# Kernel optimization log

Measured on AMD Instinct MI355X. Metric: run time of the kernel, lower is better.

Reference implementation:

```python
import jax, jax.numpy as jnp
import numpy as np

NUM_HEADS = 16
EPS = 1e-6
NEG_INF = -1e9


def layer_norm(x, scale, bias):
    m = jnp.mean(x, axis=-1, keepdims=True)
    v = jnp.mean(jnp.square(x - m), axis=-1, keepdims=True)
    return (x - m) * jax.lax.rsqrt(v + EPS) * scale + bias


def mha(x_q, x_kv, wq, wk, wv, wo, causal):
    B, Sq, D = x_q.shape
    Sk = x_kv.shape[1]
    H = NUM_HEADS
    Dh = D // H
    q = (x_q @ wq).reshape(B, Sq, H, Dh) * (1.0 / np.sqrt(Dh))
    k = (x_kv @ wk).reshape(B, Sk, H, Dh)
    v = (x_kv @ wv).reshape(B, Sk, H, Dh)
    scores = jnp.einsum('bqhf,bkhf->bhqk', q, k)  # [B,H,Sq,Sk]
    if causal:
        mask = jnp.tril(jnp.ones((Sq, Sk), dtype=bool))
        scores = jnp.where(mask, scores, NEG_INF)
    p = jax.nn.softmax(scores, axis=-1)
    o = jnp.einsum('bhqk,bkhf->bqhf', p, v).reshape(B, Sq, D)
    return o @ wo


def setup_inputs() -> dict:
    key = jax.random.key(0)
    ks = jax.random.split(key, 12)
    B, S, D, F = 2, 2048, 1024, 4096
    w = 0.02
    return {
        'targets': jax.random.normal(ks[0], (B, S, D), jnp.float32),
        'encoded': jax.random.normal(ks[1], (B, S, D), jnp.float32),
        'ln1_s': jnp.ones((D,), jnp.float32),
        'ln1_b': jnp.zeros((D,), jnp.float32),
        'sa_wq': jax.random.normal(ks[2], (D, D), jnp.float32) * w,
        'sa_wk': jax.random.normal(ks[3], (D, D), jnp.float32) * w,
        'sa_wv': jax.random.normal(ks[4], (D, D), jnp.float32) * w,
        'sa_wo': jax.random.normal(ks[5], (D, D), jnp.float32) * w,
        'ln2_s': jnp.ones((D,), jnp.float32),
        'ln2_b': jnp.zeros((D,), jnp.float32),
        'ca_wq': jax.random.normal(ks[6], (D, D), jnp.float32) * w,
        'ca_wk': jax.random.normal(ks[7], (D, D), jnp.float32) * w,
        'ca_wv': jax.random.normal(ks[8], (D, D), jnp.float32) * w,
        'ca_wo': jax.random.normal(ks[9], (D, D), jnp.float32) * w,
        'ln3_s': jnp.ones((D,), jnp.float32),
        'ln3_b': jnp.zeros((D,), jnp.float32),
        'mlp_w1': jax.random.normal(ks[10], (D, F), jnp.float32) * w,
        'mlp_b1': jnp.zeros((F,), jnp.float32),
        'mlp_w2': jax.random.normal(ks[11], (F, D), jnp.float32) * w,
        'mlp_b2': jnp.zeros((D,), jnp.float32),
    }


def reference(targets, encoded, ln1_s, ln1_b, sa_wq, sa_wk, sa_wv, sa_wo,
              ln2_s, ln2_b, ca_wq, ca_wk, ca_wv, ca_wo,
              ln3_s, ln3_b, mlp_w1, mlp_b1, mlp_w2, mlp_b2):
    # Pre-LN causal self-attention + residual
    x = layer_norm(targets, ln1_s, ln1_b)
    x = mha(x, x, sa_wq, sa_wk, sa_wv, sa_wo, causal=True)
    x = x + targets
    # Pre-LN cross-attention over encoder output + residual
    y = layer_norm(x, ln2_s, ln2_b)
    y = mha(y, encoded, ca_wq, ca_wk, ca_wv, ca_wo, causal=False)
    y = y + x
    # Pre-LN MLP + residual
    z = layer_norm(y, ln3_s, ln3_b)
    z = jax.nn.relu(z @ mlp_w1 + mlp_b1) @ mlp_w2 + mlp_b2
    return y + z
```

## Files before the change

kernel.cpp:

```cpp
#include <hip/hip_runtime.h>


#define DEV __device__ __forceinline__

typedef __attribute__((ext_vector_type(8))) _Float16 half8;
typedef __attribute__((ext_vector_type(4))) _Float16 half4;
typedef __attribute__((ext_vector_type(2))) _Float16 half2v;
typedef __attribute__((ext_vector_type(4))) float    f32x4;
typedef __attribute__((ext_vector_type(4))) unsigned int uint4v;

#define GLB(p) ((const __attribute__((address_space(1))) void*)(p))
#define LDS(p) ((__attribute__((address_space(3))) void*)(p))

DEV half2v pk(float a, float b) {
  return __builtin_bit_cast(half2v, __builtin_amdgcn_cvt_pkrtz(a, b));
}
DEV half4 pk4(float a, float b, float c, float d) {
  half2v lo = pk(a, b), hi = pk(c, d);
  half4 r; r.x = lo.x; r.y = lo.y; r.z = hi.x; r.w = hi.y;
  return r;
}

DEV float wave_sum_f(float v) {
  #pragma unroll
  for (int off = 32; off; off >>= 1) v += __shfl_xor(v, off);
  return v;
}

struct WtArgs { const float* w[8]; _Float16* wt[8]; };

__global__ __launch_bounds__(256) void wt_square(WtArgs a) {
  const float* w = a.w[blockIdx.z];
  _Float16* wt = a.wt[blockIdx.z];
  __shared__ float t[32][33];
  const int tx = threadIdx.x, ty = threadIdx.y;
  const int n0 = blockIdx.x * 32, k0 = blockIdx.y * 32;
  #pragma unroll
  for (int i = ty; i < 32; i += 8)
    t[i][tx] = w[(size_t)(k0 + i) * 1024 + n0 + tx];
  __syncthreads();
  #pragma unroll
  for (int i = ty; i < 32; i += 8)
    wt[(size_t)(n0 + i) * 1024 + k0 + tx] = (_Float16)t[tx][i];
}

__global__ __launch_bounds__(256) void wt_one(const float* __restrict__ w,
                                              _Float16* __restrict__ wt,
                                              int K, int N) {
  __shared__ float t[32][33];
  const int tx = threadIdx.x, ty = threadIdx.y;
  const int n0 = blockIdx.x * 32, k0 = blockIdx.y * 32;
  #pragma unroll
  for (int i = ty; i < 32; i += 8)
    t[i][tx] = w[(size_t)(k0 + i) * N + n0 + tx];
  __syncthreads();
  #pragma unroll
  for (int i = ty; i < 32; i += 8)
    wt[(size_t)(n0 + i) * K + k0 + tx] = (_Float16)t[tx][i];
}

__global__ __launch_bounds__(256) void cvt_f16(const float* __restrict__ in,
                                               _Float16* __restrict__ out) {
  const size_t i = ((size_t)blockIdx.x * 256 + threadIdx.x) * 4;
  const float4 v = *(const float4*)(in + i);
  *(half4*)(out + i) = pk4(v.x, v.y, v.z, v.w);
}

__global__ __launch_bounds__(256) void ln_kernel(const float* __restrict__ x,
                                                 const float* __restrict__ sc,
                                                 const float* __restrict__ bi,
                                                 _Float16* __restrict__ out) {
  const int row = blockIdx.x;
  const int t = threadIdx.x;
  const float4 v = ((const float4*)(x + (size_t)row * 1024))[t];
  float s  = v.x + v.y + v.z + v.w;
  float s2 = v.x * v.x + v.y * v.y + v.z * v.z + v.w * v.w;
  s = wave_sum_f(s); s2 = wave_sum_f(s2);
  __shared__ float red[8];
  const int lane = t & 63, wid = t >> 6;
  if (lane == 0) { red[wid] = s; red[4 + wid] = s2; }
  __syncthreads();
  s  = red[0] + red[1] + red[2] + red[3];
  s2 = red[4] + red[5] + red[6] + red[7];
  const float mean = s * (1.f / 1024.f);
  const float rstd = rsqrtf(s2 * (1.f / 1024.f) - mean * mean + 1e-6f);
  const float4 sv = ((const float4*)sc)[t];
  const float4 bv = ((const float4*)bi)[t];
  half4 o = pk4((v.x - mean) * rstd * sv.x + bv.x,
                (v.y - mean) * rstd * sv.y + bv.y,
                (v.z - mean) * rstd * sv.z + bv.z,
                (v.w - mean) * rstd * sv.w + bv.w);
  ((half4*)(out + (size_t)row * 1024))[t] = o;
}

template <int EPI, int BM, int BN, int BK>
__global__ __launch_bounds__(256)
void gemm_f16(const _Float16* __restrict__ A, const _Float16* __restrict__ Bt,
              void* __restrict__ Cout, const float* __restrict__ bias,
              const float* __restrict__ resid, int M, int N, int K,
              float scl, int sclCols, _Float16* __restrict__ vt, int vcol0) {
  constexpr int AM = BM / 32;
  constexpr int AN = BN / 32;
  constexpr int RA = BM * BK / 2048;
  constexpr int RB = BN * BK / 2048;
  constexpr int TPR = BK / 8;
  constexpr int RPR = 2048 / BK;
  constexpr int SWM = TPR - 1;
  constexpr int SH  = (TPR == 4) ? 1 : 0;
  __shared__ _Float16 As[2][BM * BK];
  __shared__ _Float16 Bs[2][BN * BK];
  const int tid = threadIdx.x;
  const int lane = tid & 63, wid = tid >> 6;
  const int wm = wid >> 1, wn = wid & 1;
  const int q = lane >> 4, m15 = lane & 15;

  const int nwg = gridDim.x * gridDim.y;
  const int bflat = blockIdx.x + gridDim.x * blockIdx.y;
  const int swz = (bflat & 7) * (nwg >> 3) + (bflat >> 3);
  const int bn = swz % gridDim.x;
  const int bm = swz / gridDim.x;

  const int trow = tid / TPR;
  const int tcolsw = ((tid % TPR) ^ ((trow >> SH) & SWM)) * 8;
  const _Float16* Ab = A + ((size_t)bm * BM + trow) * K + tcolsw;
  const _Float16* Bb = Bt + ((size_t)bn * BN + trow) * K + tcolsw;

  f32x4 acc[AM][AN] = {};

  auto stage = [&](int k0, int buf) {
    #pragma unroll
    for (int r = 0; r < RA; r++)
      __builtin_amdgcn_global_load_lds(GLB(Ab + (size_t)r * RPR * K + k0),
                                       LDS(&As[buf][r * 2048 + wid * 512]), 16, 0, 0);
    #pragma unroll
    for (int r = 0; r < RB; r++)
      __builtin_amdgcn_global_load_lds(GLB(Bb + (size_t)r * RPR * K + k0),
                                       LDS(&Bs[buf][r * 2048 + wid * 512]), 16, 0, 0);
  };

  stage(0, 0);
  const int nit = K / BK;
  for (int it = 0; it < nit; it++) {
    const int buf = it & 1;
    __syncthreads();
    if (it + 1 < nit) stage((it + 1) * BK, buf ^ 1);
    #pragma unroll
    for (int kk = 0; kk < BK / 32; kk++) {
      half8 af[AM], bf[AN];
      #pragma unroll
      for (int i = 0; i < AM; i++) {
        const int ra = wm * (BM / 2) + i * 16 + m15;
        af[i] = *(const half8*)&As[buf][ra * BK + (((kk * 4 + q) ^ ((ra >> SH) & SWM)) << 3)];
      }
      #pragma unroll
      for (int i = 0; i < AN; i++) {
        const int rb = wn * (BN / 2) + i * 16 + m15;
        bf[i] = *(const half8*)&Bs[buf][rb * BK + (((kk * 4 + q) ^ ((rb >> SH) & SWM)) << 3)];
      }
      #pragma unroll
      for (int mi = 0; mi < AM; mi++)
        #pragma unroll
        for (int ni = 0; ni < AN; ni++)
          acc[mi][ni] = __builtin_amdgcn_mfma_f32_16x16x32_f16(af[mi], bf[ni],
                                                               acc[mi][ni], 0, 0, 0);
    }
  }

  const int rowbase = bm * BM + wm * (BM / 2);
  const int colbase = bn * BN + wn * (BN / 2);
  #pragma unroll
  for (int ni = 0; ni < AN; ni++) {
    const int col = colbase + ni * 16 + m15;
    float bv = 0.f;
    if (EPI == 2 || EPI == 4) bv = bias[col];
    const float cs = (EPI == 1 || EPI == 5) ? (col < sclCols ? scl : 1.f) : 1.f;
    if (EPI == 5 && col >= vcol0) {
      const int d = col & 63, hh = (col >> 6) & 15;
      #pragma unroll
      for (int mi = 0; mi < AM; mi++) {
        const int row = rowbase + mi * 16 + q * 4;
        const int bb = row >> 11, ss = row & 2047;
        half4 ov = pk4(acc[mi][ni][0], acc[mi][ni][1],
                       acc[mi][ni][2], acc[mi][ni][3]);
        *(half4*)(vt + ((size_t)(bb * 16 + hh) * 64 + d) * 2048 + ss) = ov;
      }
      continue;
    }
    #pragma unroll
    for (int mi = 0; mi < AM; mi++) {
      #pragma unroll
      for (int r = 0; r < 4; r++) {
        const int row = rowbase + mi * 16 + q * 4 + r;
        const size_t idx = (size_t)row * N + col;
        float v = acc[mi][ni][r];
        if (EPI == 1 || EPI == 5) {
          ((_Float16*)Cout)[idx] = (_Float16)(v * cs);
        } else if (EPI == 2) {
          v += bv; v = v > 0.f ? v : 0.f;
          ((_Float16*)Cout)[idx] = (_Float16)v;
        } else if (EPI == 3) {
          ((float*)Cout)[idx] = v + resid[idx];
        } else {
          ((float*)Cout)[idx] = v + bv + resid[idx];
        }
      }
    }
  }
}

__global__ __launch_bounds__(256, 4)
void flash_attn(const _Float16* __restrict__ Q, int qs,
                const _Float16* __restrict__ Kp, int ks,
                const _Float16* __restrict__ Vt,
                _Float16* __restrict__ Opart, float* __restrict__ Lpart,
                int S, int Sk, int causal) {
  __shared__ _Float16 Ks[2][64 * 64];
  __shared__ _Float16 Vs[2][64 * 64];
  const int tid = threadIdx.x;
  const int lane = tid & 63, wid = tid >> 6;
  const int quad = lane >> 4, c15 = lane & 15;

  const int gx = gridDim.x;
  const int lid = blockIdx.x + gx * (blockIdx.y + 16 * blockIdx.z);
  const int xcd = lid & 7, slot = lid >> 3;
  const int bh = xcd * 4 + (slot / gx);
  const int qs2 = slot % gx;
  const int h = bh & 15, b = bh >> 4;
  int qb = qs2 >> 1;
  const int split = qs2 & 1;
  const int NQB = gx >> 1;
  if (causal) qb = (qb & 1) ? (NQB - 1 - (qb >> 1)) : (qb >> 1);
  const int qw0 = qb * 128 + wid * 32;

  half8 qf[2][2];
  #pragma unroll
  for (int nt = 0; nt < 2; nt++)
    #pragma unroll
    for (int kk = 0; kk < 2; kk++)
      qf[nt][kk] = *(const half8*)(Q + (size_t)(b * S + qw0 + nt * 16 + c15) * qs +
                                   h * 64 + kk * 32 + quad * 8);

  f32x4 oacc[4][2];
  #pragma unroll
  for (int i = 0; i < 4; i++)
    #pragma unroll
    for (int j = 0; j < 2; j++)
      oacc[i][j] = (f32x4){0.f, 0.f, 0.f, 0.f};
  float lpart[2] = {0.f, 0.f};

  const int ntF = causal ? (2 * qb + 2) : (Sk >> 6);
  const _Float16* Kg = Kp + (size_t)b * Sk * ks + h * 64;
  const _Float16* Vg = Vt + (size_t)(b * 16 + h) * 64 * Sk;

  const int srow8 = lane >> 3;
  const int ssw = (((lane & 7) ^ srow8) << 3);
  auto stage = [&](int jb, int buf) {
    #pragma unroll
    for (int r = 0; r < 2; r++) {
      const int row = wid * 8 + srow8 + r * 32;
      __builtin_amdgcn_global_load_lds(
          GLB(Kg + (size_t)(jb + row) * ks + ssw),
          LDS(&Ks[buf][(wid * 8 + r * 32) * 64]), 16, 0, 0);
      __builtin_amdgcn_global_load_lds(
          GLB(Vg + (size_t)row * Sk + jb + ssw),
          LDS(&Vs[buf][(wid * 8 + r * 32) * 64]), 16, 0, 0);
    }
  };

  const int t0 = split;
  stage(t0 << 6, 0);
  __syncthreads();

  const int rsw = c15 & 7;
  const int ck0 = ((quad ^ rsw) << 3);
  const int ck1 = (((quad ^ 4) ^ rsw) << 3);

  int cur = 0;
  for (int t = t0; t < ntF; t += 2) {
    const int jb = t << 6;
    if (t + 2 < ntF) stage((t + 2) << 6, cur ^ 1);

    if (!(causal && jb > qw0 + 31)) {
      f32x4 s[4][2];
      #pragma unroll
      for (int mt = 0; mt < 4; mt++) {
        const half8 kf0 = *(const half8*)&Ks[cur][(mt * 16 + c15) * 64 + ck0];
        const half8 kf1 = *(const half8*)&Ks[cur][(mt * 16 + c15) * 64 + ck1];
        #pragma unroll
        for (int nt = 0; nt < 2; nt++) {
          f32x4 z = {0.f, 0.f, 0.f, 0.f};
          z = __builtin_amdgcn_mfma_f32_16x16x32_f16(kf0, qf[nt][0], z, 0, 0, 0);
          z = __builtin_amdgcn_mfma_f32_16x16x32_f16(kf1, qf[nt][1], z, 0, 0, 0);
          s[mt][nt] = z;
        }
      }

      if (causal && jb + 63 > qw0) {
        #pragma unroll
        for (int mt = 0; mt < 4; mt++)
          #pragma unroll
          for (int nt = 0; nt < 2; nt++) {
            const int qglob = qw0 + nt * 16 + c15;
            #pragma unroll
            for (int rr = 0; rr < 4; rr++) {
              const int kglob = jb + mt * 16 + quad * 4 + rr;
              if (kglob > qglob) s[mt][nt][rr] = -1e30f;
            }
          }
      }

      unsigned int pkd[4][2][2];
      #pragma unroll
      for (int nt = 0; nt < 2; nt++) {
        float psum = 0.f;
        #pragma unroll
        for (int mt = 0; mt < 4; mt++) {
          #pragma unroll
          for (int rr = 0; rr < 4; rr++) {
            const float p = exp2f(s[mt][nt][rr]);
            s[mt][nt][rr] = p;
            psum += p;
          }
          pkd[mt][nt][0] = __builtin_bit_cast(unsigned int,
                             pk(s[mt][nt][0], s[mt][nt][1]));
          pkd[mt][nt][1] = __builtin_bit_cast(unsigned int,
                             pk(s[mt][nt][2], s[mt][nt][3]));
        }
        lpart[nt] += psum;
      }

      half8 pb[2][2];
      #pragma unroll
      for (int kk = 0; kk < 2; kk++)
        #pragma unroll
        for (int nt = 0; nt < 2; nt++) {
          unsigned int w[4];
          #pragma unroll
          for (int jd = 0; jd < 4; jd++) {
            const int src = ((quad & 1) * 2 + (jd >> 1)) * 16 + c15;
            const unsigned int xs = __shfl(pkd[2 * kk][nt][jd & 1], src);
            const unsigned int ys = __shfl(pkd[2 * kk + 1][nt][jd & 1], src);
            w[jd] = (quad & 2) ? ys : xs;
          }
          uint4v u = {w[0], w[1], w[2], w[3]};
          pb[kk][nt] = __builtin_bit_cast(half8, u);
        }

      #pragma unroll
      for (int mtd = 0; mtd < 4; mtd++) {
        const half8 vf0 = *(const half8*)&Vs[cur][(mtd * 16 + c15) * 64 + ck0];
        const half8 vf1 = *(const half8*)&Vs[cur][(mtd * 16 + c15) * 64 + ck1];
        #pragma unroll
        for (int nt = 0; nt < 2; nt++) {
          oacc[mtd][nt] = __builtin_amdgcn_mfma_f32_16x16x32_f16(vf0, pb[0][nt],
                                                                 oacc[mtd][nt], 0, 0, 0);
          oacc[mtd][nt] = __builtin_amdgcn_mfma_f32_16x16x32_f16(vf1, pb[1][nt],
                                                                 oacc[mtd][nt], 0, 0, 0);
        }
      }
    }

    __syncthreads();
    cur ^= 1;
  }

  _Float16* Ob = Opart + (size_t)split * ((size_t)2 * S * 1024) +
                 (size_t)b * S * 1024;
  #pragma unroll
  for (int nt = 0; nt < 2; nt++) {
    float l = lpart[nt];
    l += __shfl_xor(l, 16);
    l += __shfl_xor(l, 32);
    const int qrow = qw0 + nt * 16 + c15;
    if (quad == 0)
      Lpart[((size_t)(split * 2 + b) * 16 + h) * S + qrow] = l;
    #pragma unroll
    for (int mtd = 0; mtd < 4; mtd++) {
      half4 ov = pk4(oacc[mtd][nt][0], oacc[mtd][nt][1],
                     oacc[mtd][nt][2], oacc[mtd][nt][3]);
      *(half4*)(Ob + (size_t)qrow * 1024 + h * 64 + mtd * 16 + quad * 4) = ov;
    }
  }
}

__global__ __launch_bounds__(256)
void attn_combine(const _Float16* __restrict__ Op, const float* __restrict__ Lp,
                  _Float16* __restrict__ O) {
  const int row = blockIdx.x, tid = threadIdx.x;
  const int col = tid << 2, h = tid >> 4;
  const int b = row >> 11, sq = row & 2047;
  const float la = Lp[((size_t)(b * 16 + h)) * 2048 + sq];
  const float lb = Lp[((size_t)((b + 2) * 16 + h)) * 2048 + sq];
  const float linv = 1.f / (la + lb);
  const half4 pa = *(const half4*)(Op + (size_t)row * 1024 + col);
  const half4 pb = *(const half4*)(Op + ((size_t)4096 + row) * 1024 + col);
  half4 o = pk4(((float)pa.x + (float)pb.x) * linv,
                ((float)pa.y + (float)pb.y) * linv,
                ((float)pa.z + (float)pb.z) * linv,
                ((float)pa.w + (float)pb.w) * linv);
  *(half4*)(O + (size_t)row * 1024 + col) = o;
}

extern "C" void kernel_launch(void* const* d_in, const int* in_sizes, int n_in,
                              void* d_out, int out_size, void* d_ws, size_t ws_size,
                              hipStream_t stream) {
  const float* targets = (const float*)d_in[0];
  const float* encoded = (const float*)d_in[1];
  const float* ln1_s = (const float*)d_in[2];
  const float* ln1_b = (const float*)d_in[3];
  const float* sa_wq = (const float*)d_in[4];
  const float* sa_wk = (const float*)d_in[5];
  const float* sa_wv = (const float*)d_in[6];
  const float* sa_wo = (const float*)d_in[7];
  const float* ln2_s = (const float*)d_in[8];
  const float* ln2_b = (const float*)d_in[9];
  const float* ca_wq = (const float*)d_in[10];
  const float* ca_wk = (const float*)d_in[11];
  const float* ca_wv = (const float*)d_in[12];
  const float* ca_wo = (const float*)d_in[13];
  const float* ln3_s = (const float*)d_in[14];
  const float* ln3_b = (const float*)d_in[15];
  const float* mlp_w1 = (const float*)d_in[16];
  const float* mlp_b1 = (const float*)d_in[17];
  const float* mlp_w2 = (const float*)d_in[18];
  const float* mlp_b2 = (const float*)d_in[19];

  const int B = 2, S = 2048, D = 1024, F = 4096, M = B * S;
  const size_t MB = 1024ull * 1024ull;
  const float QSCALE = 0.125f * 1.44269504f;
  char* ws = (char*)d_ws;
  _Float16* wsq   = (_Float16*)(ws);
  _Float16* w1t   = (_Float16*)(ws + 16 * MB);
  _Float16* w2t   = (_Float16*)(ws + 24 * MB);
  _Float16* Abf   = (_Float16*)(ws + 32 * MB);
  _Float16* encbf = (_Float16*)(ws + 40 * MB);
  _Float16* QKV   = (_Float16*)(ws + 48 * MB);
  _Float16* Qcb   = (_Float16*)(ws + 48 * MB);
  _Float16* KVb   = (_Float16*)(ws + 56 * MB);
  _Float16* h1    = (_Float16*)(ws + 48 * MB);
  float*    Lbuf  = (float*)(ws + 72 * MB);
  _Float16* Vtb   = (_Float16*)(ws + 80 * MB);
  _Float16* Aob   = (_Float16*)(ws + 88 * MB);
  float*    xres  = (float*)(ws + 96 * MB);
  float*    yres  = (float*)(ws + 112 * MB);
  _Float16* Opart = (_Float16*)(ws + 112 * MB);

  {
    WtArgs wa;
    const float* sw[8] = {sa_wq, sa_wk, sa_wv, sa_wo, ca_wq, ca_wk, ca_wv, ca_wo};
    for (int i = 0; i < 8; i++) { wa.w[i] = sw[i]; wa.wt[i] = wsq + (size_t)i * D * D; }
    wt_square<<<dim3(32, 32, 8), dim3(32, 8), 0, stream>>>(wa);
  }
  wt_one<<<dim3(F / 32, D / 32), dim3(32, 8), 0, stream>>>(mlp_w1, w1t, D, F);
  wt_one<<<dim3(D / 32, F / 32), dim3(32, 8), 0, stream>>>(mlp_w2, w2t, F, D);
  cvt_f16<<<(M * D) / 1024, 256, 0, stream>>>(encoded, encbf);

  const dim3 gA(2 * (S / 128), 16, B);

  ln_kernel<<<M, 256, 0, stream>>>(targets, ln1_s, ln1_b, Abf);
  gemm_f16<5, 128, 128, 32><<<dim3(3072 / 128, M / 128), 256, 0, stream>>>(
      Abf, wsq, QKV, nullptr, nullptr, M, 3072, D, QSCALE, 1024, Vtb, 2048);
  flash_attn<<<gA, 256, 0, stream>>>(QKV, 3072, QKV + 1024, 3072, Vtb,
                                     Opart, Lbuf, S, S, 1);
  attn_combine<<<M, 256, 0, stream>>>(Opart, Lbuf, Aob);
  gemm_f16<3, 64, 64, 64><<<dim3(1024 / 64, M / 64), 256, 0, stream>>>(
      Aob, wsq + 3ull * D * D, xres, nullptr, targets, M, D, D, 1.f, 0, nullptr, 0);

  ln_kernel<<<M, 256, 0, stream>>>(xres, ln2_s, ln2_b, Abf);
  gemm_f16<1, 64, 64, 64><<<dim3(1024 / 64, M / 64), 256, 0, stream>>>(
      Abf, wsq + 4ull * D * D, Qcb, nullptr, nullptr, M, D, D, QSCALE, 1024, nullptr, 0);
  gemm_f16<5, 64, 128, 32><<<dim3(2048 / 128, M / 64), 256, 0, stream>>>(
      encbf, wsq + 5ull * D * D, KVb, nullptr, nullptr, M, 2048, D, 1.f, 0, Vtb, 1024);
  flash_attn<<<gA, 256, 0, stream>>>(Qcb, 1024, KVb, 2048, Vtb,
                                     Opart, Lbuf, S, S, 0);
  attn_combine<<<M, 256, 0, stream>>>(Opart, Lbuf, Aob);
  gemm_f16<3, 64, 64, 64><<<dim3(1024 / 64, M / 64), 256, 0, stream>>>(
      Aob, wsq + 7ull * D * D, yres, nullptr, xres, M, D, D, 1.f, 0, nullptr, 0);

  ln_kernel<<<M, 256, 0, stream>>>(yres, ln3_s, ln3_b, Abf);
  gemm_f16<2, 128, 128, 32><<<dim3(F / 128, M / 128), 256, 0, stream>>>(
      Abf, w1t, h1, mlp_b1, nullptr, M, F, D, 1.f, 0, nullptr, 0);
  gemm_f16<4, 64, 64, 64><<<dim3(1024 / 64, M / 64), 256, 0, stream>>>(
      h1, w2t, (float*)d_out, mlp_b2, yres, M, D, F, 1.f, 0, nullptr, 0);

  (void)in_sizes; (void)n_in; (void)out_size; (void)ws_size;
}
```

Baseline: 540.2 us.

## Use 512-thread attention blocks with 256-row query tiles and three-way KV split

```diff
diff --git a/kernel.cpp b/kernel.cpp
--- a/kernel.cpp
+++ b/kernel.cpp
@@ -208,11 +208,12 @@
   }
 }
 
-__global__ __launch_bounds__(256, 4)
+__global__ __launch_bounds__(512, 6)
 void flash_attn(const _Float16* __restrict__ Q, int qs,
                 const _Float16* __restrict__ Kp, int ks,
                 const _Float16* __restrict__ Vt,
-                _Float16* __restrict__ Opart, float* __restrict__ Lpart,
+                _Float16* __restrict__ Op01, _Float16* __restrict__ Op2,
+                float* __restrict__ Lpart,
                 int S, int Sk, int causal) {
   __shared__ _Float16 Ks[2][64 * 64];
   __shared__ _Float16 Vs[2][64 * 64];
@@ -226,11 +227,11 @@
   const int bh = xcd * 4 + (slot / gx);
   const int qs2 = slot % gx;
   const int h = bh & 15, b = bh >> 4;
-  int qb = qs2 >> 1;
-  const int split = qs2 & 1;
-  const int NQB = gx >> 1;
+  int qb = qs2 / 3;
+  const int split = qs2 % 3;
+  const int NQB = gx / 3;
   if (causal) qb = (qb & 1) ? (NQB - 1 - (qb >> 1)) : (qb >> 1);
-  const int qw0 = qb * 128 + wid * 32;
+  const int qw0 = qb * 256 + wid * 32;
 
   half8 qf[2][2];
   #pragma unroll
@@ -248,23 +249,19 @@
       oacc[i][j] = (f32x4){0.f, 0.f, 0.f, 0.f};
   float lpart[2] = {0.f, 0.f};
 
-  const int ntF = causal ? (2 * qb + 2) : (Sk >> 6);
+  const int ntF = causal ? (4 * qb + 4) : (Sk >> 6);
   const _Float16* Kg = Kp + (size_t)b * Sk * ks + h * 64;
   const _Float16* Vg = Vt + (size_t)(b * 16 + h) * 64 * Sk;
 
-  const int srow8 = lane >> 3;
-  const int ssw = (((lane & 7) ^ srow8) << 3);
+  const int srow = tid >> 3;
+  const int ssw = (((tid & 7) ^ (srow & 7)) << 3);
   auto stage = [&](int jb, int buf) {
-    #pragma unroll
-    for (int r = 0; r < 2; r++) {
-      const int row = wid * 8 + srow8 + r * 32;
-      __builtin_amdgcn_global_load_lds(
-          GLB(Kg + (size_t)(jb + row) * ks + ssw),
-          LDS(&Ks[buf][(wid * 8 + r * 32) * 64]), 16, 0, 0);
-      __builtin_amdgcn_global_load_lds(
-          GLB(Vg + (size_t)row * Sk + jb + ssw),
-          LDS(&Vs[buf][(wid * 8 + r * 32) * 64]), 16, 0, 0);
-    }
+    __builtin_amdgcn_global_load_lds(
+        GLB(Kg + (size_t)(jb + srow) * ks + ssw),
+        LDS(&Ks[buf][(wid * 8) * 64]), 16, 0, 0);
+    __builtin_amdgcn_global_load_lds(
+        GLB(Vg + (size_t)srow * Sk + jb + ssw),
+        LDS(&Vs[buf][(wid * 8) * 64]), 16, 0, 0);
   };
 
   const int t0 = split;
@@ -276,9 +273,9 @@
   const int ck1 = (((quad ^ 4) ^ rsw) << 3);
 
   int cur = 0;
-  for (int t = t0; t < ntF; t += 2) {
+  for (int t = t0; t < ntF; t += 3) {
     const int jb = t << 6;
-    if (t + 2 < ntF) stage((t + 2) << 6, cur ^ 1);
+    if (t + 3 < ntF) stage((t + 3) << 6, cur ^ 1);
 
     if (!(causal && jb > qw0 + 31)) {
       f32x4 s[4][2];
@@ -364,8 +361,9 @@
     cur ^= 1;
   }
 
-  _Float16* Ob = Opart + (size_t)split * ((size_t)2 * S * 1024) +
-                 (size_t)b * S * 1024;
+  _Float16* Ob = (split < 2)
+      ? Op01 + (size_t)split * ((size_t)2 * S * 1024) + (size_t)b * S * 1024
+      : Op2 + (size_t)b * S * 1024;
   #pragma unroll
   for (int nt = 0; nt < 2; nt++) {
     float l = lpart[nt];
@@ -384,20 +382,23 @@
 }
 
 __global__ __launch_bounds__(256)
-void attn_combine(const _Float16* __restrict__ Op, const float* __restrict__ Lp,
-                  _Float16* __restrict__ O) {
+void attn_combine(const _Float16* __restrict__ Op01,
+                  const _Float16* __restrict__ Op2,
+                  const float* __restrict__ Lp, _Float16* __restrict__ O) {
   const int row = blockIdx.x, tid = threadIdx.x;
   const int col = tid << 2, h = tid >> 4;
   const int b = row >> 11, sq = row & 2047;
   const float la = Lp[((size_t)(b * 16 + h)) * 2048 + sq];
-  const float lb = Lp[((size_t)((b + 2) * 16 + h)) * 2048 + sq];
-  const float linv = 1.f / (la + lb);
-  const half4 pa = *(const half4*)(Op + (size_t)row * 1024 + col);
-  const half4 pb = *(const half4*)(Op + ((size_t)4096 + row) * 1024 + col);
-  half4 o = pk4(((float)pa.x + (float)pb.x) * linv,
-                ((float)pa.y + (float)pb.y) * linv,
-                ((float)pa.z + (float)pb.z) * linv,
-                ((float)pa.w + (float)pb.w) * linv);
+  const float lb = Lp[((size_t)((2 + b) * 16 + h)) * 2048 + sq];
+  const float lc = Lp[((size_t)((4 + b) * 16 + h)) * 2048 + sq];
+  const float linv = 1.f / (la + lb + lc);
+  const half4 pa = *(const half4*)(Op01 + (size_t)row * 1024 + col);
+  const half4 pbv = *(const half4*)(Op01 + ((size_t)4096 + row) * 1024 + col);
+  const half4 pc = *(const half4*)(Op2 + (size_t)row * 1024 + col);
+  half4 o = pk4(((float)pa.x + (float)pbv.x + (float)pc.x) * linv,
+                ((float)pa.y + (float)pbv.y + (float)pc.y) * linv,
+                ((float)pa.z + (float)pbv.z + (float)pc.z) * linv,
+                ((float)pa.w + (float)pbv.w + (float)pc.w) * linv);
   *(half4*)(O + (size_t)row * 1024 + col) = o;
 }
 
@@ -444,6 +445,7 @@
   float*    xres  = (float*)(ws + 96 * MB);
   float*    yres  = (float*)(ws + 112 * MB);
   _Float16* Opart = (_Float16*)(ws + 112 * MB);
+  _Float16* Opt2  = Abf;
 
   {
     WtArgs wa;
@@ -455,14 +457,14 @@
   wt_one<<<dim3(D / 32, F / 32), dim3(32, 8), 0, stream>>>(mlp_w2, w2t, F, D);
   cvt_f16<<<(M * D) / 1024, 256, 0, stream>>>(encoded, encbf);
 
-  const dim3 gA(2 * (S / 128), 16, B);
+  const dim3 gA(3 * (S / 256), 16, B);
 
   ln_kernel<<<M, 256, 0, stream>>>(targets, ln1_s, ln1_b, Abf);
   gemm_f16<5, 128, 128, 32><<<dim3(3072 / 128, M / 128), 256, 0, stream>>>(
       Abf, wsq, QKV, nullptr, nullptr, M, 3072, D, QSCALE, 1024, Vtb, 2048);
-  flash_attn<<<gA, 256, 0, stream>>>(QKV, 3072, QKV + 1024, 3072, Vtb,
-                                     Opart, Lbuf, S, S, 1);
-  attn_combine<<<M, 256, 0, stream>>>(Opart, Lbuf, Aob);
+  flash_attn<<<gA, 512, 0, stream>>>(QKV, 3072, QKV + 1024, 3072, Vtb,
+                                     Opart, Opt2, Lbuf, S, S, 1);
+  attn_combine<<<M, 256, 0, stream>>>(Opart, Opt2, Lbuf, Aob);
   gemm_f16<3, 64, 64, 64><<<dim3(1024 / 64, M / 64), 256, 0, stream>>>(
       Aob, wsq + 3ull * D * D, xres, nullptr, targets, M, D, D, 1.f, 0, nullptr, 0);
 
@@ -471,9 +473,9 @@
       Abf, wsq + 4ull * D * D, Qcb, nullptr, nullptr, M, D, D, QSCALE, 1024, nullptr, 0);
   gemm_f16<5, 64, 128, 32><<<dim3(2048 / 128, M / 64), 256, 0, stream>>>(
       encbf, wsq + 5ull * D * D, KVb, nullptr, nullptr, M, 2048, D, 1.f, 0, Vtb, 1024);
-  flash_attn<<<gA, 256, 0, stream>>>(Qcb, 1024, KVb, 2048, Vtb,
-                                     Opart, Lbuf, S, S, 0);
-  attn_combine<<<M, 256, 0, stream>>>(Opart, Lbuf, Aob);
+  flash_attn<<<gA, 512, 0, stream>>>(Qcb, 1024, KVb, 2048, Vtb,
+                                     Opart, Opt2, Lbuf, S, S, 0);
+  attn_combine<<<M, 256, 0, stream>>>(Opart, Opt2, Lbuf, Aob);
   gemm_f16<3, 64, 64, 64><<<dim3(1024 / 64, M / 64), 256, 0, stream>>>(
       Aob, wsq + 7ull * D * D, yres, nullptr, xres, M, D, D, 1.f, 0, nullptr, 0);
 
```

After: 765.5 us. +41.7%, slower.
